# Performance work log

Hardware: AMD Instinct MI355X
Metric: run time of the kernel (lower is better)

## Reference

```python
import jax, jax.numpy as jnp
import numpy as np

D = 768      # embed_dim
L = 12       # depth
NH = 12      # num_heads
HS = D // NH # head_size = 64
HID = 4 * D  # mlp hidden = 3072
EPS = 1e-5


def setup_inputs() -> dict:
    key = jax.random.key(0)
    ks = jax.random.split(key, 6)
    std = 0.02
    # fix_init_weight rescale: proj.weight and fc2.weight divided by sqrt(2*layer_id)
    rescale = 1.0 / jnp.sqrt(2.0 * jnp.arange(1, L + 1, dtype=jnp.float32))[:, None, None]
    inp = {
        "x": jax.random.normal(ks[0], (2, 1024, D), jnp.float32),
        "Wqkv": jax.random.normal(ks[1], (L, 3 * D, D), jnp.float32) * std,
        "bqkv": jnp.zeros((L, 3 * D), jnp.float32),
        "Wproj": jax.random.normal(ks[2], (L, D, D), jnp.float32) * std * rescale,
        "bproj": jnp.zeros((L, D), jnp.float32),
        "W1": jax.random.normal(ks[3], (L, HID, D), jnp.float32) * std,
        "b1": jnp.zeros((L, HID), jnp.float32),
        "W2": jax.random.normal(ks[4], (L, D, HID), jnp.float32) * std * rescale,
        "b2": jnp.zeros((L, D), jnp.float32),
        "ln1w": jnp.ones((L, D), jnp.float32),
        "ln1b": jnp.zeros((L, D), jnp.float32),
        "ln2w": jnp.ones((L, D), jnp.float32),
        "ln2b": jnp.zeros((L, D), jnp.float32),
        "lnw": jnp.ones((D,), jnp.float32),
        "lnb": jnp.zeros((D,), jnp.float32),
    }
    return inp


def _layernorm(x, w, b):
    mu = x.mean(-1, keepdims=True)
    var = ((x - mu) ** 2).mean(-1, keepdims=True)
    return (x - mu) / jnp.sqrt(var + EPS) * w + b


def _sincos_pos_embed(n, d):
    # get_1d_sincos_pos_embed: omega = 1/10000**(arange(d/2)/(d/2))
    omega = 1.0 / (10000.0 ** (jnp.arange(d // 2, dtype=jnp.float32) / (d / 2.0)))
    out = jnp.arange(n, dtype=jnp.float32)[:, None] * omega[None, :]  # [n, d/2]
    return jnp.concatenate([jnp.sin(out), jnp.cos(out)], axis=1)      # [n, d]


def _forward(x, Wqkv, bqkv, Wproj, bproj, W1, b1, W2, b2,
             ln1w, ln1b, ln2w, ln2b, lnw, lnb):
    b, n, d = x.shape
    x = x + _sincos_pos_embed(n, d)[None]
    scale = HS ** -0.5

    def block(x, p):
        wqkv, bq, wp, bp, w1, b1_, w2, b2_, l1w, l1b, l2w, l2b = p
        # pre-norm attention (mask=False -> plain softmax attention)
        h = _layernorm(x, l1w, l1b)
        qkv = h @ wqkv.T + bq                                   # [b, n, 3d]
        qkv = qkv.reshape(b, n, 3, NH, HS).transpose(2, 0, 3, 1, 4)
        q, k, v = qkv[0], qkv[1], qkv[2]                        # [b, nh, n, hs]
        att = jax.nn.softmax(scale * jnp.einsum('bhqd,bhkd->bhqk', q, k), axis=-1)
        o = jnp.einsum('bhqk,bhkd->bhqd', att, v)               # [b, nh, n, hs]
        o = o.transpose(0, 2, 1, 3).reshape(b, n, d)
        x = x + (o @ wp.T + bp)
        # pre-norm MLP (exact GELU, as nn.GELU default)
        h2 = _layernorm(x, l2w, l2b)
        y = jax.nn.gelu(h2 @ w1.T + b1_, approximate=False) @ w2.T + b2_
        return x + y, None

    x, _ = jax.lax.scan(block, x,
                        (Wqkv, bqkv, Wproj, bproj, W1, b1, W2, b2,
                         ln1w, ln1b, ln2w, ln2b))
    return _layernorm(x, lnw, lnb)


def reference(x, Wqkv, bqkv, Wproj, bproj, W1, b1, W2, b2,
              ln1w, ln1b, ln2w, ln2b, lnw, lnb):
    return _forward(x, Wqkv, bqkv, Wproj, bproj, W1, b1, W2, b2,
                    ln1w, ln1b, ln2w, ln2b, lnw, lnb)
```

## Files before the change

kernel.cpp:

```cpp
#include <hip/hip_runtime.h>
#include <math.h>

#define NTOK 2048
#define DM 768
#define NHD 12
#define HS 64
#define SEQ 1024
#define HID 3072
#define NL 12

typedef __attribute__((ext_vector_type(8))) short short8;
typedef __attribute__((ext_vector_type(4))) float f32x4;
typedef __attribute__((ext_vector_type(4))) unsigned short us4;
typedef unsigned short u16;

static __device__ __forceinline__ u16 f2bf(float f) {
    unsigned u = __float_as_uint(f);
    u = (u + 0x7fffu + ((u >> 16) & 1u)) >> 16;
    return (u16)u;
}

static __device__ __forceinline__ void gload16(const void* g, void* l) {
    __builtin_amdgcn_global_load_lds(
        (const __attribute__((address_space(1))) void*)g,
        (__attribute__((address_space(3))) void*)l,
        16, 0, 0);
}

__global__ void posadd_k(const float* __restrict__ xin, float* __restrict__ xout) {
    int idx = blockIdx.x * 256 + threadIdx.x;
    int d = idx % DM;
    int tok = (idx / DM) & (SEQ - 1);
    int i = (d < 384) ? d : d - 384;
    float omega = expf((float)i * (-9.210340371976184f / 384.0f));
    float ang = (float)tok * omega;
    float pe = (d < 384) ? sinf(ang) : cosf(ang);
    xout[idx] = xin[idx] + pe;
}

__global__ void cvt_k(const float* __restrict__ in, u16* __restrict__ out) {
    int idx = blockIdx.x * 256 + threadIdx.x;
    float4 f = ((const float4*)in)[idx];
    us4 u = { f2bf(f.x), f2bf(f.y), f2bf(f.z), f2bf(f.w) };
    ((us4*)out)[idx] = u;
}

template<bool OUTBF>
__global__ __launch_bounds__(256) void ln_k(
        const float* __restrict__ x, const float* __restrict__ w,
        const float* __restrict__ b, void* __restrict__ out) {
    int l = threadIdx.x & 63, wv = threadIdx.x >> 6;
    int row = blockIdx.x * 4 + wv;
    const float* xr = x + (size_t)row * DM;
    float4 v[3];
#pragma unroll
    for (int c = 0; c < 3; c++) v[c] = *(const float4*)(xr + c * 256 + l * 4);
    float s = 0.f;
#pragma unroll
    for (int c = 0; c < 3; c++) s += v[c].x + v[c].y + v[c].z + v[c].w;
#pragma unroll
    for (int off = 32; off; off >>= 1) s += __shfl_xor(s, off, 64);
    float mu = s * (1.0f / DM);
    float vs = 0.f;
#pragma unroll
    for (int c = 0; c < 3; c++) {
        float dx;
        dx = v[c].x - mu; vs += dx * dx;
        dx = v[c].y - mu; vs += dx * dx;
        dx = v[c].z - mu; vs += dx * dx;
        dx = v[c].w - mu; vs += dx * dx;
    }
#pragma unroll
    for (int off = 32; off; off >>= 1) vs += __shfl_xor(vs, off, 64);
    float rstd = rsqrtf(vs * (1.0f / DM) + 1e-5f);
#pragma unroll
    for (int c = 0; c < 3; c++) {
        float4 w4 = *(const float4*)(w + c * 256 + l * 4);
        float4 b4 = *(const float4*)(b + c * 256 + l * 4);
        float y0 = (v[c].x - mu) * rstd * w4.x + b4.x;
        float y1 = (v[c].y - mu) * rstd * w4.y + b4.y;
        float y2 = (v[c].z - mu) * rstd * w4.z + b4.z;
        float y3 = (v[c].w - mu) * rstd * w4.w + b4.w;
        if (OUTBF) {
            us4 u = { f2bf(y0), f2bf(y1), f2bf(y2), f2bf(y3) };
            *(us4*)((u16*)out + (size_t)row * DM + c * 256 + l * 4) = u;
        } else {
            float4 o4 = { y0, y1, y2, y3 };
            *(float4*)((float*)out + (size_t)row * DM + c * 256 + l * 4) = o4;
        }
    }
}

template<int BM, int BN, int WR, int WC, int MODE>
__global__ __launch_bounds__(512) void gemm_k(
        const u16* __restrict__ A, const u16* __restrict__ B,
        const float* __restrict__ bias, int K,
        float* __restrict__ xres, u16* __restrict__ o0, u16* __restrict__ o1,
        u16* __restrict__ o2) {
    constexpr int WM = BM / WR, WN = BN / WC;
    constexpr int FM = WM / 16, FN = WN / 16;
    constexpr int ACH = BM / 64, BCH = BN / 64;

    __shared__ u16 lA[2][BM * 64];
    __shared__ u16 lB[2][BN * 64];
    const char* Ab = (const char*)A;
    const char* Bb = (const char*)B;

    int tid = threadIdx.x;
    int l = tid & 63, w = tid >> 6;
    int lr = l & 15, lg = l >> 4;
    int wr = w / WC, wc = w % WC;
    int bm = blockIdx.y * BM;
    int bn = blockIdx.x * BN;

    auto stage = [&](int buf, int kk) {
#pragma unroll
        for (int c = 0; c < ACH; c++) {
            int p = (c * 512 + tid) * 16;
            int row = p >> 7, kb = p & 127;
            int kbs = kb ^ ((row & 7) << 4);
            gload16(Ab + ((size_t)(bm + row) * K + kk) * 2 + kbs, (char*)lA[buf] + p);
        }
#pragma unroll
        for (int c = 0; c < BCH; c++) {
            int p = (c * 512 + tid) * 16;
            int row = p >> 7, kb = p & 127;
            int kbs = kb ^ ((row & 7) << 4);
            gload16(Bb + ((size_t)(bn + row) * K + kk) * 2 + kbs, (char*)lB[buf] + p);
        }
    };

    f32x4 acc[FM][FN] = {};

    stage(0, 0);
    __syncthreads();
    int cur = 0;
    for (int kk = 0; kk < K; kk += 64) {
        if (kk + 64 < K) stage(cur ^ 1, kk + 64);
        const char* lAb = (const char*)lA[cur];
        const char* lBb = (const char*)lB[cur];
#pragma unroll
        for (int ks = 0; ks < 2; ks++) {
            short8 af[FM], bf[FN];
#pragma unroll
            for (int i = 0; i < FM; i++) {
                int row = wr * WM + i * 16 + lr;
                int kb = ks * 64 + lg * 16;
                af[i] = *(const short8*)(lAb + row * 128 + (kb ^ ((row & 7) << 4)));
            }
#pragma unroll
            for (int j = 0; j < FN; j++) {
                int row = wc * WN + j * 16 + lr;
                int kb = ks * 64 + lg * 16;
                bf[j] = *(const short8*)(lBb + row * 128 + (kb ^ ((row & 7) << 4)));
            }
#pragma unroll
            for (int i = 0; i < FM; i++)
#pragma unroll
                for (int j = 0; j < FN; j++)
                    acc[i][j] = __builtin_amdgcn_mfma_f32_16x16x32_bf16(af[i], bf[j], acc[i][j], 0, 0, 0);
        }
        __syncthreads();
        cur ^= 1;
    }

#pragma unroll
    for (int i = 0; i < FM; i++)
#pragma unroll
        for (int j = 0; j < FN; j++)
#pragma unroll
            for (int r = 0; r < 4; r++) {
                int gm = bm + wr * WM + i * 16 + lg * 4 + r;
                int gn = bn + wc * WN + j * 16 + lr;
                float v = acc[i][j][r] + bias[gn];
                if (MODE == 0) {
                    int bi = gm >> 10, tok = gm & (SEQ - 1);
                    int which = gn / DM;
                    int wi = gn - which * DM;
                    int h = wi >> 6, d = wi & 63;
                    if (which == 0)      o0[(((size_t)bi * NHD + h) * SEQ + tok) * HS + d] = f2bf(v * 0.125f);
                    else if (which == 1) o1[(((size_t)bi * NHD + h) * SEQ + tok) * HS + d] = f2bf(v);
                    else                 o2[(((size_t)bi * NHD + h) * HS + d) * SEQ + tok] = f2bf(v);
                } else if (MODE == 1) {
                    size_t ix = (size_t)gm * DM + gn;
                    xres[ix] += v;
                } else {
                    float g = 0.5f * v * (1.0f + erff(v * 0.70710678f));
                    o0[(size_t)gm * HID + gn] = f2bf(g);
                }
            }
}

__global__ __launch_bounds__(256) void attn_k(
        const u16* __restrict__ q, const u16* __restrict__ k,
        const u16* __restrict__ vtg, u16* __restrict__ o) {
    __shared__ u16 kt[2][64 * 64];
    __shared__ u16 vtile[2][64 * 64];
    __shared__ u16 plds[4][16][72];

    int tid = threadIdx.x;
    int l = tid & 63, w = tid >> 6;
    int lr = l & 15, lg = l >> 4;
    int bh = blockIdx.y;
    int bi = bh / NHD, h = bh - bi * NHD;
    int qbase = blockIdx.x * 64 + w * 16;

    const u16* qp = q + (size_t)bh * SEQ * HS;
    const char* kp = (const char*)(k + (size_t)bh * SEQ * HS);
    const char* vp = (const char*)(vtg + (size_t)bh * HS * SEQ);

    short8 aq[2];
#pragma unroll
    for (int c = 0; c < 2; c++)
        aq[c] = *(const short8*)(qp + (size_t)(qbase + lr) * HS + c * 32 + lg * 8);

    auto stage = [&](int buf, int kb) {
#pragma unroll
        for (int c = 0; c < 2; c++) {
            int p = (c * 256 + tid) * 16;
            int row = p >> 7, db = p & 127;
            int dbs = db ^ ((row & 7) << 4);
            gload16(kp + (size_t)(kb + row) * 128 + dbs, (char*)kt[buf] + p);
        }
#pragma unroll
        for (int c = 0; c < 2; c++) {
            int p = (c * 256 + tid) * 16;
            int row = p >> 7, db = p & 127;
            int dbs = db ^ ((row & 7) << 4);
            gload16(vp + (size_t)row * (SEQ * 2) + kb * 2 + dbs, (char*)vtile[buf] + p);
        }
    };

    float mrow[4], lsum[4];
#pragma unroll
    for (int r = 0; r < 4; r++) { mrow[r] = -1e30f; lsum[r] = 0.f; }
    f32x4 oacc[4] = {};

    stage(0, 0);
    __syncthreads();
    int buf = 0;
    for (int kb = 0; kb < SEQ; kb += 64) {
        if (kb + 64 < SEQ) stage(buf ^ 1, kb + 64);
        const char* kb_ = (const char*)kt[buf];
        const char* vb_ = (const char*)vtile[buf];

        f32x4 s[4];
#pragma unroll
        for (int t = 0; t < 4; t++) {
            f32x4 st = {};
#pragma unroll
            for (int c = 0; c < 2; c++) {
                int row = t * 16 + lr;
                short8 bk = *(const short8*)(kb_ + row * 128 + ((c * 64 + lg * 16) ^ ((row & 7) << 4)));
                st = __builtin_amdgcn_mfma_f32_16x16x32_bf16(aq[c], bk, st, 0, 0, 0);
            }
            s[t] = st;
        }

        float e[4][4], scl[4];
#pragma unroll
        for (int r = 0; r < 4; r++) {
            float mx = fmaxf(fmaxf(s[0][r], s[1][r]), fmaxf(s[2][r], s[3][r]));
#pragma unroll
            for (int off = 8; off; off >>= 1) mx = fmaxf(mx, __shfl_xor(mx, off, 16));
            float mnew = fmaxf(mrow[r], mx);
            float sc = __expf(mrow[r] - mnew);
            float ss = 0.f;
#pragma unroll
            for (int t = 0; t < 4; t++) { e[t][r] = __expf(s[t][r] - mnew); ss += e[t][r]; }
#pragma unroll
            for (int off = 8; off; off >>= 1) ss += __shfl_xor(ss, off, 16);
            lsum[r] = lsum[r] * sc + ss;
            mrow[r] = mnew;
            scl[r] = sc;
        }
#pragma unroll
        for (int j = 0; j < 4; j++)
#pragma unroll
            for (int r = 0; r < 4; r++) oacc[j][r] *= scl[r];

#pragma unroll
        for (int t = 0; t < 4; t++)
#pragma unroll
            for (int r = 0; r < 4; r++)
                plds[w][lg * 4 + r][t * 16 + lr] = f2bf(e[t][r]);
        short8 pa[2];
#pragma unroll
        for (int kc = 0; kc < 2; kc++)
            pa[kc] = *(const short8*)(&plds[w][lr][kc * 32 + lg * 8]);

#pragma unroll
        for (int j = 0; j < 4; j++) {
            int row = j * 16 + lr;
#pragma unroll
            for (int kc = 0; kc < 2; kc++) {
                short8 bv = *(const short8*)(vb_ + row * 128 + ((kc * 64 + lg * 16) ^ ((row & 7) << 4)));
                oacc[j] = __builtin_amdgcn_mfma_f32_16x16x32_bf16(pa[kc], bv, oacc[j], 0, 0, 0);
            }
        }
        __syncthreads();
        buf ^= 1;
    }

#pragma unroll
    for (int j = 0; j < 4; j++)
#pragma unroll
        for (int r = 0; r < 4; r++) {
            int qrow = qbase + lg * 4 + r;
            float v = oacc[j][r] / lsum[r];
            o[((size_t)bi * SEQ + qrow) * DM + h * HS + j * 16 + lr] = f2bf(v);
        }
}

extern "C" void kernel_launch(void* const* d_in, const int* in_sizes, int n_in,
                              void* d_out, int out_size, void* d_ws, size_t ws_size,
                              hipStream_t stream) {
    const float* x_in  = (const float*)d_in[0];
    const float* Wqkv  = (const float*)d_in[1];
    const float* bqkv  = (const float*)d_in[2];
    const float* Wproj = (const float*)d_in[3];
    const float* bproj = (const float*)d_in[4];
    const float* W1    = (const float*)d_in[5];
    const float* b1    = (const float*)d_in[6];
    const float* W2    = (const float*)d_in[7];
    const float* b2    = (const float*)d_in[8];
    const float* ln1w  = (const float*)d_in[9];
    const float* ln1b  = (const float*)d_in[10];
    const float* ln2w  = (const float*)d_in[11];
    const float* ln2b  = (const float*)d_in[12];
    const float* lnw   = (const float*)d_in[13];
    const float* lnb   = (const float*)d_in[14];

    char* ws = (char*)d_ws;
    size_t off = 0;
    auto alloc = [&](size_t bytes) -> void* {
        void* p = ws + off;
        off += (bytes + 255) & ~(size_t)255;
        return p;
    };
    float* xbuf = (float*)alloc((size_t)NTOK * DM * 4);
    u16* hbuf   = (u16*)alloc((size_t)NTOK * DM * 2);
    u16* qb     = (u16*)alloc((size_t)2 * NHD * SEQ * HS * 2);
    u16* kb     = (u16*)alloc((size_t)2 * NHD * SEQ * HS * 2);
    u16* vtb    = (u16*)alloc((size_t)2 * NHD * SEQ * HS * 2);
    u16* ob     = (u16*)alloc((size_t)NTOK * DM * 2);
    u16* h2b    = (u16*)alloc((size_t)NTOK * HID * 2);

    const size_t nWqkv  = (size_t)NL * 3 * DM * DM;
    const size_t nWproj = (size_t)NL * DM * DM;
    const size_t nW1    = (size_t)NL * HID * DM;
    const size_t nW2    = (size_t)NL * DM * HID;
    size_t wbytes = (nWqkv + nWproj + nW1 + nW2) * 2 + 4 * 256;
    bool wb = (off + wbytes) <= ws_size;

    u16 *wqkvh = nullptr, *wprojh = nullptr, *w1h = nullptr, *w2h = nullptr;
    u16 *cvtbuf = nullptr;
    if (wb) {
        wqkvh  = (u16*)alloc(nWqkv * 2);
        wprojh = (u16*)alloc(nWproj * 2);
        w1h    = (u16*)alloc(nW1 * 2);
        w2h    = (u16*)alloc(nW2 * 2);
    } else {
        cvtbuf = (u16*)alloc((size_t)HID * DM * 2);
    }

    posadd_k<<<dim3((NTOK * DM) / 256), 256, 0, stream>>>(x_in, xbuf);
    if (wb) {
        cvt_k<<<dim3((unsigned)(nWqkv / 4 / 256)), 256, 0, stream>>>(Wqkv, wqkvh);
        cvt_k<<<dim3((unsigned)(nWproj / 4 / 256)), 256, 0, stream>>>(Wproj, wprojh);
        cvt_k<<<dim3((unsigned)(nW1 / 4 / 256)), 256, 0, stream>>>(W1, w1h);
        cvt_k<<<dim3((unsigned)(nW2 / 4 / 256)), 256, 0, stream>>>(W2, w2h);
    }

    for (int l = 0; l < NL; l++) {
        const u16* wqkv_l;
        const u16* wproj_l;
        const u16* w1_l;
        const u16* w2_l;

        ln_k<true><<<dim3(NTOK / 4), 256, 0, stream>>>(xbuf, ln1w + l * DM, ln1b + l * DM, hbuf);

        if (wb) wqkv_l = wqkvh + (size_t)l * 3 * DM * DM;
        else {
            cvt_k<<<dim3(3 * DM * DM / 1024), 256, 0, stream>>>(Wqkv + (size_t)l * 3 * DM * DM, cvtbuf);
            wqkv_l = cvtbuf;
        }
        gemm_k<128, 128, 2, 4, 0><<<dim3(3 * DM / 128, NTOK / 128), 512, 0, stream>>>(
            hbuf, wqkv_l, bqkv + (size_t)l * 3 * DM, DM, nullptr, qb, kb, vtb);

        attn_k<<<dim3(SEQ / 64, 24), 256, 0, stream>>>(qb, kb, vtb, ob);

        if (wb) wproj_l = wprojh + (size_t)l * DM * DM;
        else {
            cvt_k<<<dim3(DM * DM / 1024), 256, 0, stream>>>(Wproj + (size_t)l * DM * DM, cvtbuf);
            wproj_l = cvtbuf;
        }
        gemm_k<128, 64, 4, 2, 1><<<dim3(DM / 64, NTOK / 128), 512, 0, stream>>>(
            ob, wproj_l, bproj + (size_t)l * DM, DM, xbuf, nullptr, nullptr, nullptr);

        ln_k<true><<<dim3(NTOK / 4), 256, 0, stream>>>(xbuf, ln2w + l * DM, ln2b + l * DM, hbuf);

        if (wb) w1_l = w1h + (size_t)l * HID * DM;
        else {
            cvt_k<<<dim3(HID * DM / 1024), 256, 0, stream>>>(W1 + (size_t)l * HID * DM, cvtbuf);
            w1_l = cvtbuf;
        }
        gemm_k<128, 128, 2, 4, 2><<<dim3(HID / 128, NTOK / 128), 512, 0, stream>>>(
            hbuf, w1_l, b1 + (size_t)l * HID, DM, nullptr, h2b, nullptr, nullptr);

        if (wb) w2_l = w2h + (size_t)l * DM * HID;
        else {
            cvt_k<<<dim3(DM * HID / 1024), 256, 0, stream>>>(W2 + (size_t)l * DM * HID, cvtbuf);
            w2_l = cvtbuf;
        }
        gemm_k<128, 64, 4, 2, 1><<<dim3(DM / 64, NTOK / 128), 512, 0, stream>>>(
            h2b, w2_l, b2 + (size_t)l * DM, HID, xbuf, nullptr, nullptr, nullptr);
    }

    ln_k<false><<<dim3(NTOK / 4), 256, 0, stream>>>(xbuf, lnw, lnb, (float*)d_out);
}
```

Measured before the change: 1.888 ms.

## Fuse pre-norm layernorm into QKV and FC1 GEMM A-tile loading

```diff
diff --git a/kernel.cpp b/kernel.cpp
--- a/kernel.cpp
+++ b/kernel.cpp
@@ -91,20 +91,22 @@
     }
 }
 
-template<int BM, int BN, int WR, int WC, int MODE>
-__global__ __launch_bounds__(512) void gemm_k(
-        const u16* __restrict__ A, const u16* __restrict__ B,
+template<int BM, int BN, int NT, int WR, int WC, int MODE, bool ALN>
+__global__ __launch_bounds__(NT) void gemm_k(
+        const void* __restrict__ Ap, const u16* __restrict__ B,
         const float* __restrict__ bias, int K,
+        const float* __restrict__ lnw, const float* __restrict__ lnb,
         float* __restrict__ xres, u16* __restrict__ o0, u16* __restrict__ o1,
         u16* __restrict__ o2) {
     constexpr int WM = BM / WR, WN = BN / WC;
     constexpr int FM = WM / 16, FN = WN / 16;
-    constexpr int ACH = BM / 64, BCH = BN / 64;
+    constexpr int ACH = (BM * 128) / (NT * 16);
+    constexpr int BCH = (BN * 128) / (NT * 16);
 
     __shared__ u16 lA[2][BM * 64];
     __shared__ u16 lB[2][BN * 64];
-    const char* Ab = (const char*)A;
-    const char* Bb = (const char*)B;
+    __shared__ float smu[BM];
+    __shared__ float srs[BM];
 
     int tid = threadIdx.x;
     int l = tid & 63, w = tid >> 6;
@@ -113,30 +115,77 @@
     int bm = blockIdx.y * BM;
     int bn = blockIdx.x * BN;
 
-    auto stage = [&](int buf, int kk) {
+    if constexpr (ALN) {
+        constexpr int TPR = NT / BM;
+        constexpr int NIT = DM / 4 / TPR;
+        int row = tid / TPR, c4 = tid % TPR;
+        const float4* xr4 = (const float4*)((const float*)Ap + (size_t)(bm + row) * DM);
+        float s = 0.f, q = 0.f;
+#pragma unroll 8
+        for (int i = 0; i < NIT; i++) {
+            float4 v = xr4[i * TPR + c4];
+            s += v.x + v.y + v.z + v.w;
+            q += v.x * v.x + v.y * v.y + v.z * v.z + v.w * v.w;
+        }
+        s += __shfl_xor(s, 1, 64); s += __shfl_xor(s, 2, 64);
+        q += __shfl_xor(q, 1, 64); q += __shfl_xor(q, 2, 64);
+        if (c4 == 0) {
+            float mu = s * (1.0f / DM);
+            smu[row] = mu;
+            srs[row] = rsqrtf(q * (1.0f / DM) - mu * mu + 1e-5f);
+        }
+        __syncthreads();
+    }
+
+    auto stageA = [&](int buf, int kk) {
 #pragma unroll
         for (int c = 0; c < ACH; c++) {
-            int p = (c * 512 + tid) * 16;
-            int row = p >> 7, kb = p & 127;
-            int kbs = kb ^ ((row & 7) << 4);
-            gload16(Ab + ((size_t)(bm + row) * K + kk) * 2 + kbs, (char*)lA[buf] + p);
-        }
+            int p = (c * NT + tid) * 16;
+            int row = p >> 7, cb = p & 127;
+            int cbs = cb ^ ((row & 7) << 4);
+            if constexpr (ALN) {
+                const float* src = (const float*)Ap + (size_t)(bm + row) * DM + kk + (cbs >> 1);
+                float4 f0 = ((const float4*)src)[0];
+                float4 f1 = ((const float4*)src)[1];
+                const float4* wp = (const float4*)(lnw + kk + (cbs >> 1));
+                const float4* bp = (const float4*)(lnb + kk + (cbs >> 1));
+                float4 w0 = wp[0], w1 = wp[1];
+                float4 b0 = bp[0], b1 = bp[1];
+                float mu = smu[row], rs = srs[row];
+                short8 t;
+                t[0] = (short)f2bf((f0.x - mu) * rs * w0.x + b0.x);
+                t[1] = (short)f2bf((f0.y - mu) * rs * w0.y + b0.y);
+                t[2] = (short)f2bf((f0.z - mu) * rs * w0.z + b0.z);
+                t[3] = (short)f2bf((f0.w - mu) * rs * w0.w + b0.w);
+                t[4] = (short)f2bf((f1.x - mu) * rs * w1.x + b1.x);
+                t[5] = (short)f2bf((f1.y - mu) * rs * w1.y + b1.y);
+                t[6] = (short)f2bf((f1.z - mu) * rs * w1.z + b1.z);
+                t[7] = (short)f2bf((f1.w - mu) * rs * w1.w + b1.w);
+                *(short8*)((char*)lA[buf] + p) = t;
+            } else {
+                gload16((const char*)Ap + ((size_t)(bm + row) * K + kk) * 2 + cbs,
+                        (char*)lA[buf] + p);
+            }
+        }
+    };
+    auto stageB = [&](int buf, int kk) {
 #pragma unroll
         for (int c = 0; c < BCH; c++) {
-            int p = (c * 512 + tid) * 16;
-            int row = p >> 7, kb = p & 127;
-            int kbs = kb ^ ((row & 7) << 4);
-            gload16(Bb + ((size_t)(bn + row) * K + kk) * 2 + kbs, (char*)lB[buf] + p);
+            int p = (c * NT + tid) * 16;
+            int row = p >> 7, cb = p & 127;
+            int cbs = cb ^ ((row & 7) << 4);
+            gload16((const char*)B + ((size_t)(bn + row) * K + kk) * 2 + cbs,
+                    (char*)lB[buf] + p);
         }
     };
 
     f32x4 acc[FM][FN] = {};
 
-    stage(0, 0);
+    stageA(0, 0); stageB(0, 0);
     __syncthreads();
     int cur = 0;
     for (int kk = 0; kk < K; kk += 64) {
-        if (kk + 64 < K) stage(cur ^ 1, kk + 64);
+        if (kk + 64 < K) { stageA(cur ^ 1, kk + 64); stageB(cur ^ 1, kk + 64); }
         const char* lAb = (const char*)lA[cur];
         const char* lBb = (const char*)lB[cur];
 #pragma unroll
@@ -339,7 +388,6 @@
         return p;
     };
     float* xbuf = (float*)alloc((size_t)NTOK * DM * 4);
-    u16* hbuf   = (u16*)alloc((size_t)NTOK * DM * 2);
     u16* qb     = (u16*)alloc((size_t)2 * NHD * SEQ * HS * 2);
     u16* kb     = (u16*)alloc((size_t)2 * NHD * SEQ * HS * 2);
     u16* vtb    = (u16*)alloc((size_t)2 * NHD * SEQ * HS * 2);
@@ -378,15 +426,14 @@
         const u16* w1_l;
         const u16* w2_l;
 
-        ln_k<true><<<dim3(NTOK / 4), 256, 0, stream>>>(xbuf, ln1w + l * DM, ln1b + l * DM, hbuf);
-
         if (wb) wqkv_l = wqkvh + (size_t)l * 3 * DM * DM;
         else {
             cvt_k<<<dim3(3 * DM * DM / 1024), 256, 0, stream>>>(Wqkv + (size_t)l * 3 * DM * DM, cvtbuf);
             wqkv_l = cvtbuf;
         }
-        gemm_k<128, 128, 2, 4, 0><<<dim3(3 * DM / 128, NTOK / 128), 512, 0, stream>>>(
-            hbuf, wqkv_l, bqkv + (size_t)l * 3 * DM, DM, nullptr, qb, kb, vtb);
+        gemm_k<128, 64, 512, 4, 2, 0, true><<<dim3(3 * DM / 64, NTOK / 128), 512, 0, stream>>>(
+            xbuf, wqkv_l, bqkv + (size_t)l * 3 * DM, DM,
+            ln1w + l * DM, ln1b + l * DM, nullptr, qb, kb, vtb);
 
         attn_k<<<dim3(SEQ / 64, 24), 256, 0, stream>>>(qb, kb, vtb, ob);
 
@@ -395,26 +442,27 @@
             cvt_k<<<dim3(DM * DM / 1024), 256, 0, stream>>>(Wproj + (size_t)l * DM * DM, cvtbuf);
             wproj_l = cvtbuf;
         }
-        gemm_k<128, 64, 4, 2, 1><<<dim3(DM / 64, NTOK / 128), 512, 0, stream>>>(
-            ob, wproj_l, bproj + (size_t)l * DM, DM, xbuf, nullptr, nullptr, nullptr);
-
-        ln_k<true><<<dim3(NTOK / 4), 256, 0, stream>>>(xbuf, ln2w + l * DM, ln2b + l * DM, hbuf);
+        gemm_k<64, 64, 256, 2, 2, 1, false><<<dim3(DM / 64, NTOK / 64), 256, 0, stream>>>(
+            ob, wproj_l, bproj + (size_t)l * DM, DM,
+            nullptr, nullptr, xbuf, nullptr, nullptr, nullptr);
 
         if (wb) w1_l = w1h + (size_t)l * HID * DM;
         else {
             cvt_k<<<dim3(HID * DM / 1024), 256, 0, stream>>>(W1 + (size_t)l * HID * DM, cvtbuf);
             w1_l = cvtbuf;
         }
-        gemm_k<128, 128, 2, 4, 2><<<dim3(HID / 128, NTOK / 128), 512, 0, stream>>>(
-            hbuf, w1_l, b1 + (size_t)l * HID, DM, nullptr, h2b, nullptr, nullptr);
+        gemm_k<128, 64, 512, 4, 2, 2, true><<<dim3(HID / 64, NTOK / 128), 512, 0, stream>>>(
+            xbuf, w1_l, b1 + (size_t)l * HID, DM,
+            ln2w + l * DM, ln2b + l * DM, nullptr, h2b, nullptr, nullptr);
 
         if (wb) w2_l = w2h + (size_t)l * DM * HID;
         else {
             cvt_k<<<dim3(DM * HID / 1024), 256, 0, stream>>>(W2 + (size_t)l * DM * HID, cvtbuf);
             w2_l = cvtbuf;
         }
-        gemm_k<128, 64, 4, 2, 1><<<dim3(DM / 64, NTOK / 128), 512, 0, stream>>>(
-            h2b, w2_l, b2 + (size_t)l * DM, HID, xbuf, nullptr, nullptr, nullptr);
+        gemm_k<64, 64, 256, 2, 2, 1, false><<<dim3(DM / 64, NTOK / 64), 256, 0, stream>>>(
+            h2b, w2_l, b2 + (size_t)l * DM, HID,
+            nullptr, nullptr, xbuf, nullptr, nullptr, nullptr);
     }
 
     ln_k<false><<<dim3(NTOK / 4), 256, 0, stream>>>(xbuf, lnw, lnb, (float*)d_out);
```

New measurement: 2.352 ms. +24.6%, slower.

## Triple-buffer GEMM LDS staging with vmcnt waits and smaller tiles for N=768 GEMMs

Applied to the files above, without the earlier changes.

```diff
diff --git a/kernel.cpp b/kernel.cpp
--- a/kernel.cpp
+++ b/kernel.cpp
@@ -25,6 +25,13 @@
         (const __attribute__((address_space(1))) void*)g,
         (__attribute__((address_space(3))) void*)l,
         16, 0, 0);
+}
+
+template<int N> static __device__ __forceinline__ void waitvm() {
+    if constexpr (N == 0)      asm volatile("s_waitcnt vmcnt(0)" ::: "memory");
+    else if constexpr (N == 4) asm volatile("s_waitcnt vmcnt(4)" ::: "memory");
+    else if constexpr (N == 8) asm volatile("s_waitcnt vmcnt(8)" ::: "memory");
+    else static_assert(N == 0 || N == 4 || N == 8, "unsupported vmcnt");
 }
 
 __global__ void posadd_k(const float* __restrict__ xin, float* __restrict__ xout) {
@@ -91,18 +98,20 @@
     }
 }
 
-template<int BM, int BN, int WR, int WC, int MODE>
-__global__ __launch_bounds__(512) void gemm_k(
+template<int BM, int BN, int NT, int WR, int WC, int MODE>
+__global__ __launch_bounds__(NT) void gemm_k(
         const u16* __restrict__ A, const u16* __restrict__ B,
         const float* __restrict__ bias, int K,
         float* __restrict__ xres, u16* __restrict__ o0, u16* __restrict__ o1,
         u16* __restrict__ o2) {
     constexpr int WM = BM / WR, WN = BN / WC;
     constexpr int FM = WM / 16, FN = WN / 16;
-    constexpr int ACH = BM / 64, BCH = BN / 64;
-
-    __shared__ u16 lA[2][BM * 64];
-    __shared__ u16 lB[2][BN * 64];
+    constexpr int ACH = (BM * 128) / (NT * 16);
+    constexpr int BCH = (BN * 128) / (NT * 16);
+    constexpr int L = ACH + BCH;
+
+    __shared__ u16 lA[3][BM * 64];
+    __shared__ u16 lB[3][BN * 64];
     const char* Ab = (const char*)A;
     const char* Bb = (const char*)B;
 
@@ -116,29 +125,32 @@
     auto stage = [&](int buf, int kk) {
 #pragma unroll
         for (int c = 0; c < ACH; c++) {
-            int p = (c * 512 + tid) * 16;
-            int row = p >> 7, kb = p & 127;
-            int kbs = kb ^ ((row & 7) << 4);
-            gload16(Ab + ((size_t)(bm + row) * K + kk) * 2 + kbs, (char*)lA[buf] + p);
+            int p = (c * NT + tid) * 16;
+            int row = p >> 7, cb = p & 127;
+            int cbs = cb ^ ((row & 7) << 4);
+            gload16(Ab + ((size_t)(bm + row) * K + kk) * 2 + cbs, (char*)lA[buf] + p);
         }
 #pragma unroll
         for (int c = 0; c < BCH; c++) {
-            int p = (c * 512 + tid) * 16;
-            int row = p >> 7, kb = p & 127;
-            int kbs = kb ^ ((row & 7) << 4);
-            gload16(Bb + ((size_t)(bn + row) * K + kk) * 2 + kbs, (char*)lB[buf] + p);
+            int p = (c * NT + tid) * 16;
+            int row = p >> 7, cb = p & 127;
+            int cbs = cb ^ ((row & 7) << 4);
+            gload16(Bb + ((size_t)(bn + row) * K + kk) * 2 + cbs, (char*)lB[buf] + p);
         }
     };
 
     f32x4 acc[FM][FN] = {};
 
+    int nt = K / 64;
     stage(0, 0);
-    __syncthreads();
-    int cur = 0;
-    for (int kk = 0; kk < K; kk += 64) {
-        if (kk + 64 < K) stage(cur ^ 1, kk + 64);
-        const char* lAb = (const char*)lA[cur];
-        const char* lBb = (const char*)lB[cur];
+    stage(1, 64);
+    for (int t = 0; t < nt; ++t) {
+        if (t + 1 < nt) waitvm<L>(); else waitvm<0>();
+        __builtin_amdgcn_s_barrier();
+        if (t + 2 < nt) stage((t + 2) % 3, (t + 2) * 64);
+        int b = t % 3;
+        const char* lAb = (const char*)lA[b];
+        const char* lBb = (const char*)lB[b];
 #pragma unroll
         for (int ks = 0; ks < 2; ks++) {
             short8 af[FM], bf[FN];
@@ -160,8 +172,6 @@
                 for (int j = 0; j < FN; j++)
                     acc[i][j] = __builtin_amdgcn_mfma_f32_16x16x32_bf16(af[i], bf[j], acc[i][j], 0, 0, 0);
         }
-        __syncthreads();
-        cur ^= 1;
     }
 
 #pragma unroll
@@ -385,7 +395,7 @@
             cvt_k<<<dim3(3 * DM * DM / 1024), 256, 0, stream>>>(Wqkv + (size_t)l * 3 * DM * DM, cvtbuf);
             wqkv_l = cvtbuf;
         }
-        gemm_k<128, 128, 2, 4, 0><<<dim3(3 * DM / 128, NTOK / 128), 512, 0, stream>>>(
+        gemm_k<128, 128, 512, 2, 4, 0><<<dim3(3 * DM / 128, NTOK / 128), 512, 0, stream>>>(
             hbuf, wqkv_l, bqkv + (size_t)l * 3 * DM, DM, nullptr, qb, kb, vtb);
 
         attn_k<<<dim3(SEQ / 64, 24), 256, 0, stream>>>(qb, kb, vtb, ob);
@@ -395,7 +405,7 @@
             cvt_k<<<dim3(DM * DM / 1024), 256, 0, stream>>>(Wproj + (size_t)l * DM * DM, cvtbuf);
             wproj_l = cvtbuf;
         }
-        gemm_k<128, 64, 4, 2, 1><<<dim3(DM / 64, NTOK / 128), 512, 0, stream>>>(
+        gemm_k<64, 64, 256, 2, 2, 1><<<dim3(DM / 64, NTOK / 64), 256, 0, stream>>>(
             ob, wproj_l, bproj + (size_t)l * DM, DM, xbuf, nullptr, nullptr, nullptr);
 
         ln_k<true><<<dim3(NTOK / 4), 256, 0, stream>>>(xbuf, ln2w + l * DM, ln2b + l * DM, hbuf);
@@ -405,7 +415,7 @@
             cvt_k<<<dim3(HID * DM / 1024), 256, 0, stream>>>(W1 + (size_t)l * HID * DM, cvtbuf);
             w1_l = cvtbuf;
         }
-        gemm_k<128, 128, 2, 4, 2><<<dim3(HID / 128, NTOK / 128), 512, 0, stream>>>(
+        gemm_k<128, 128, 512, 2, 4, 2><<<dim3(HID / 128, NTOK / 128), 512, 0, stream>>>(
             hbuf, w1_l, b1 + (size_t)l * HID, DM, nullptr, h2b, nullptr, nullptr);
 
         if (wb) w2_l = w2h + (size_t)l * DM * HID;
@@ -413,7 +423,7 @@
             cvt_k<<<dim3(DM * HID / 1024), 256, 0, stream>>>(W2 + (size_t)l * DM * HID, cvtbuf);
             w2_l = cvtbuf;
         }
-        gemm_k<128, 64, 4, 2, 1><<<dim3(DM / 64, NTOK / 128), 512, 0, stream>>>(
+        gemm_k<64, 64, 256, 2, 2, 1><<<dim3(DM / 64, NTOK / 64), 256, 0, stream>>>(
             h2b, w2_l, b2 + (size_t)l * DM, HID, xbuf, nullptr, nullptr, nullptr);
     }
 
```

New measurement: 2.029 ms. 7.4% more time.

## Split attention over two KV halves and merge partials in a combine kernel

Applied to the files above, without the earlier changes.

```diff
diff --git a/kernel.cpp b/kernel.cpp
--- a/kernel.cpp
+++ b/kernel.cpp
@@ -193,7 +193,8 @@
 
 __global__ __launch_bounds__(256) void attn_k(
         const u16* __restrict__ q, const u16* __restrict__ k,
-        const u16* __restrict__ vtg, u16* __restrict__ o) {
+        const u16* __restrict__ vtg, float* __restrict__ Of,
+        float* __restrict__ ml) {
     __shared__ u16 kt[2][64 * 64];
     __shared__ u16 vtile[2][64 * 64];
     __shared__ u16 plds[4][16][72];
@@ -202,8 +203,9 @@
     int l = tid & 63, w = tid >> 6;
     int lr = l & 15, lg = l >> 4;
     int bh = blockIdx.y;
-    int bi = bh / NHD, h = bh - bi * NHD;
+    int half = blockIdx.z;
     int qbase = blockIdx.x * 64 + w * 16;
+    int kv0 = half * (SEQ / 2);
 
     const u16* qp = q + (size_t)bh * SEQ * HS;
     const char* kp = (const char*)(k + (size_t)bh * SEQ * HS);
@@ -236,11 +238,11 @@
     for (int r = 0; r < 4; r++) { mrow[r] = -1e30f; lsum[r] = 0.f; }
     f32x4 oacc[4] = {};
 
-    stage(0, 0);
+    stage(0, kv0);
     __syncthreads();
     int buf = 0;
-    for (int kb = 0; kb < SEQ; kb += 64) {
-        if (kb + 64 < SEQ) stage(buf ^ 1, kb + 64);
+    for (int kb = kv0; kb < kv0 + SEQ / 2; kb += 64) {
+        if (kb + 64 < kv0 + SEQ / 2) stage(buf ^ 1, kb + 64);
         const char* kb_ = (const char*)kt[buf];
         const char* vb_ = (const char*)vtile[buf];
 
@@ -302,14 +304,45 @@
         buf ^= 1;
     }
 
+    size_t pbase = ((size_t)(bh * 2 + half) * SEQ);
 #pragma unroll
     for (int j = 0; j < 4; j++)
 #pragma unroll
         for (int r = 0; r < 4; r++) {
             int qrow = qbase + lg * 4 + r;
-            float v = oacc[j][r] / lsum[r];
-            o[((size_t)bi * SEQ + qrow) * DM + h * HS + j * 16 + lr] = f2bf(v);
-        }
+            Of[(pbase + qrow) * 64 + j * 16 + lr] = oacc[j][r];
+        }
+    if (lr == 0) {
+#pragma unroll
+        for (int r = 0; r < 4; r++) {
+            int qrow = qbase + lg * 4 + r;
+            ((float2*)ml)[pbase + qrow] = make_float2(mrow[r], lsum[r]);
+        }
+    }
+}
+
+__global__ __launch_bounds__(256) void attncomb_k(
+        const float* __restrict__ Of, const float* __restrict__ ml,
+        u16* __restrict__ o) {
+    int gid = blockIdx.x * 256 + threadIdx.x;
+    int row = gid >> 4;
+    int dc = (gid & 15) * 4;
+    int bh = row >> 10, qrow = row & 1023;
+    int bi = bh / NHD, h = bh - bi * NHD;
+    const float2* mlp = (const float2*)ml;
+    float2 ml0 = mlp[(size_t)(bh * 2 + 0) * SEQ + qrow];
+    float2 ml1 = mlp[(size_t)(bh * 2 + 1) * SEQ + qrow];
+    float m = fmaxf(ml0.x, ml1.x);
+    float e0 = __expf(ml0.x - m), e1 = __expf(ml1.x - m);
+    float rl = 1.0f / (ml0.y * e0 + ml1.y * e1);
+    float4 o0 = *(const float4*)(Of + ((size_t)(bh * 2 + 0) * SEQ + qrow) * 64 + dc);
+    float4 o1 = *(const float4*)(Of + ((size_t)(bh * 2 + 1) * SEQ + qrow) * 64 + dc);
+    us4 u;
+    u[0] = f2bf((o0.x * e0 + o1.x * e1) * rl);
+    u[1] = f2bf((o0.y * e0 + o1.y * e1) * rl);
+    u[2] = f2bf((o0.z * e0 + o1.z * e1) * rl);
+    u[3] = f2bf((o0.w * e0 + o1.w * e1) * rl);
+    *(us4*)(o + ((size_t)(bi * SEQ + qrow) * DM) + h * HS + dc) = u;
 }
 
 extern "C" void kernel_launch(void* const* d_in, const int* in_sizes, int n_in,
@@ -345,6 +378,8 @@
     u16* vtb    = (u16*)alloc((size_t)2 * NHD * SEQ * HS * 2);
     u16* ob     = (u16*)alloc((size_t)NTOK * DM * 2);
     u16* h2b    = (u16*)alloc((size_t)NTOK * HID * 2);
+    float* Of   = (float*)alloc((size_t)24 * 2 * SEQ * 64 * 4);
+    float* mlb  = (float*)alloc((size_t)24 * 2 * SEQ * 8);
 
     const size_t nWqkv  = (size_t)NL * 3 * DM * DM;
     const size_t nWproj = (size_t)NL * DM * DM;
@@ -388,7 +423,8 @@
         gemm_k<128, 128, 2, 4, 0><<<dim3(3 * DM / 128, NTOK / 128), 512, 0, stream>>>(
             hbuf, wqkv_l, bqkv + (size_t)l * 3 * DM, DM, nullptr, qb, kb, vtb);
 
-        attn_k<<<dim3(SEQ / 64, 24), 256, 0, stream>>>(qb, kb, vtb, ob);
+        attn_k<<<dim3(SEQ / 64, 24, 2), 256, 0, stream>>>(qb, kb, vtb, Of, mlb);
+        attncomb_k<<<dim3(24 * SEQ * 16 / 256), 256, 0, stream>>>(Of, mlb, ob);
 
         if (wb) wproj_l = wprojh + (size_t)l * DM * DM;
         else {
```

Result: faster. 1.813 ms (-4.0%).
